# Optimization experiments

Hardware: AMD Instinct MI355X
Metric: run time of the kernel (lower is better)

## Reference

```python
import jax, jax.numpy as jnp
import numpy as np

B, P, C, H, W = 256, 512, 512, 7, 8
T = H * W  # 56
EPS = 1e-8


def setup_inputs() -> dict:
    key = jax.random.key(0)
    k1, k2, k3 = jax.random.split(key, 3)
    inp = jax.random.normal(k1, (B, C, H, W), dtype=jnp.float32)
    # xavier-uniform-like init for prototype (fan over last two dims as torch does)
    bound_p = float(np.sqrt(6.0 / (P + C * T)))
    prototype = jax.random.uniform(k2, (P, C, T), dtype=jnp.float32, minval=-bound_p, maxval=bound_p)
    bound_w = float(np.sqrt(6.0 / (C + 1)))
    fc_w = jax.random.uniform(k3, (1, C), dtype=jnp.float32, minval=-bound_w, maxval=bound_w)
    fc_b = jnp.zeros((1,), dtype=jnp.float32)
    return {"input": inp, "prototype": prototype, "fc_w": fc_w, "fc_b": fc_b}


def reference(input, prototype, fc_w, fc_b):
    # flatten spatial dims: (B, C, T)
    x = input.reshape(input.shape[0], input.shape[1], -1)
    # per-position cosine similarity over channel dim
    dots = jnp.einsum('bct,pct->bpt', x, prototype)          # (B, P, T)
    xn = jnp.linalg.norm(x, axis=1)                           # (B, T)
    pn = jnp.linalg.norm(prototype, axis=1)                   # (P, T)
    sim = dots / jnp.maximum(xn[:, None, :] * pn[None, :, :], EPS)
    att = jax.nn.softmax(sim, axis=-1)                        # (B, P, T)
    # attention-pooled elementwise product: (B, P, C)
    feat = jnp.einsum('bpt,bct,pct->bpc', att, x, prototype)
    # fc: Linear(C, 1) then relu, view to (B, P)
    out = jax.nn.relu(jnp.einsum('bpc,oc->bpo', feat, fc_w) + fc_b)
    return out.reshape(out.shape[0], out.shape[1])
```

## Files before the change

kernel.cpp:

```cpp
#include <hip/hip_runtime.h>
#include <hip/hip_bf16.h>
#include <math.h>

constexpr int kB = 256, kC = 512, kT = 56, kP = 512;
constexpr int kCT = kC * kT;

typedef short v4s __attribute__((ext_vector_type(4)));
typedef short v8s __attribute__((ext_vector_type(8)));
typedef float v4f __attribute__((ext_vector_type(4)));
typedef float v16f __attribute__((ext_vector_type(16)));

__device__ __forceinline__ unsigned pack_bf16(float a, float b) {
  __hip_bfloat16 ha = __float2bfloat16(a);
  __hip_bfloat16 hb = __float2bfloat16(b);
  unsigned short ua, ub;
  __builtin_memcpy(&ua, &ha, 2);
  __builtin_memcpy(&ub, &hb, 2);
  return (unsigned)ua | ((unsigned)ub << 16);
}

__device__ __forceinline__ v4s frag2(unsigned w0, unsigned w1) {
  unsigned u[2] = {w0, w1};
  v4s s;
  __builtin_memcpy(&s, u, 8);
  return s;
}

__device__ __forceinline__ v8s frag8(uint4 u) {
  v8s s;
  __builtin_memcpy(&s, &u, 16);
  return s;
}

__device__ __forceinline__ unsigned cvtpk(float lo, float hi) {
  unsigned r;
  asm("v_cvt_pk_bf16_f32 %0, %1, %2" : "=v"(r) : "v"(lo), "v"(hi));
  return r;
}

#define GLOAD(gp, lp)                                                        \
  __builtin_amdgcn_global_load_lds(                                          \
      (const __attribute__((address_space(1))) unsigned*)(const unsigned*)(gp), \
      (__attribute__((address_space(3))) unsigned*)(unsigned*)(lp), 16, 0, 0)


__global__ __launch_bounds__(512) void prep_kernel(
    const float* __restrict__ x, const float* __restrict__ proto,
    const float* __restrict__ fcw,
    unsigned* __restrict__ xt, unsigned* __restrict__ xwt,
    unsigned* __restrict__ pt,
    float* __restrict__ xn2, float* __restrict__ pn2) {
  __shared__ float tile[128 * 64];
  __shared__ float normp[56 * 16];

  const int tid = threadIdx.x;
  const int n = blockIdx.x;
  const bool isx = (n < kB);
  const int row = isx ? n : (n - kB);
  const float* src = (isx ? x : proto) + (size_t)row * kCT;
  const int R = isx ? kB : kP;
  unsigned* dst0 = isx ? xt : pt;

  const int l = tid & 63;
  const int w = tid >> 6;
  const int j = l & 15;
  const int tq = l >> 4;

  float na0 = 0.f, na1 = 0.f;

#pragma unroll 1
  for (int ch = 0; ch < 4; ++ch) {
    const float* csrc = src + ch * (128 * 56);

    float fw[8];
    if (isx) {
      const float* gf = fcw + ch * 128 + 8 * j;
#pragma unroll
      for (int i = 0; i < 8; ++i) fw[i] = gf[i];
    }

#pragma unroll
    for (int it = 0; it < 4; ++it) {
      const int idx = it * 512 + tid;
      if (idx < 1792) {
        const int f0 = idx * 4;
        const int c = (int)(((unsigned)f0 * 74899u) >> 22);
        const int t = f0 - c * 56;
        const int sw = ((((unsigned)c >> 3) ^ (unsigned)c) & 7) << 2;
        float4 v = *(const float4*)(csrc + f0);
        *(float4*)(tile + c * 64 + (t ^ sw)) = v;
      }
    }
    __syncthreads();

#pragma unroll
    for (int pass = 0; pass < 2; ++pass) {
      const int t = pass * 32 + w * 4 + tq;
      if (t < 56) {
        float f[8];
#pragma unroll
        for (int i = 0; i < 8; ++i) {
          const int sw = ((j ^ i) & 7) << 2;
          f[i] = tile[(8 * j + i) * 64 + (t ^ sw)];
        }
        float s = 0.f;
#pragma unroll
        for (int i = 0; i < 8; ++i) s = fmaf(f[i], f[i], s);
        if (pass == 0) na0 += s; else na1 += s;
        uint4 wx;
        wx.x = cvtpk(f[0], f[1]);
        wx.y = cvtpk(f[2], f[3]);
        wx.z = cvtpk(f[4], f[5]);
        wx.w = cvtpk(f[6], f[7]);
        const size_t o = (size_t)(t >> 2) * ((size_t)R * 1024) +
                         (size_t)row * 1024 + ch * 256 + (t & 3) * 64 + 4 * j;
        *(uint4*)(dst0 + o) = wx;
        if (isx) {
          uint4 ww;
          ww.x = cvtpk(f[0] * fw[0], f[1] * fw[1]);
          ww.y = cvtpk(f[2] * fw[2], f[3] * fw[3]);
          ww.z = cvtpk(f[4] * fw[4], f[5] * fw[5]);
          ww.w = cvtpk(f[6] * fw[6], f[7] * fw[7]);
          *(uint4*)(xwt + o) = ww;
        }
      }
    }
    __syncthreads();
  }

  {
    const int t0 = w * 4 + tq;
    normp[t0 * 16 + j] = na0;
    const int t1 = 32 + w * 4 + tq;
    if (t1 < 56) normp[t1 * 16 + j] = na1;
  }
  __syncthreads();
  if (tid < 56) {
    float s = 0.f;
#pragma unroll
    for (int k = 0; k < 16; ++k) s += normp[tid * 16 + k];
    if (isx) xn2[row * 56 + tid] = s;
    else     pn2[row * 56 + tid] = s;
  }
}

constexpr int TILE = 64 * 32;
constexpr int BUF = 3 * TILE;

__global__ __launch_bounds__(256, 2) void proto_gemm_kernel(
    const unsigned* __restrict__ xt, const unsigned* __restrict__ xwt,
    const unsigned* __restrict__ pt,
    const float* __restrict__ xn2, const float* __restrict__ pn2,
    float* __restrict__ part) {
  __shared__ __align__(16) unsigned lds[3 * BUF];
  __shared__ float xnL[4 * 64], pnL[4 * 64];

  const int tid = threadIdx.x;
  const int l = tid & 63;
  const int w4 = tid >> 6;
  const int wm = w4 >> 1;
  const int wn = w4 & 1;

  int bid = (int)blockIdx.x;
  bid = (bid & 7) * 56 + (bid >> 3);
  const int b0 = (bid & 3) * 64;
  const int p0 = ((bid >> 2) & 7) * 64;
  const int tg = bid >> 5;

  {
    const int tl = tid >> 6, r = tid & 63;
    xnL[tid] = sqrtf(xn2[(b0 + r) * 56 + tg * 4 + tl]);
    pnL[tid] = sqrtf(pn2[(p0 + r) * 56 + tg * 4 + tl]);
  }
  __syncthreads();

  const int lrow = l >> 3, lch = l & 7;
  size_t xsrc[2], psrc[2];
  int ldst[2];
#pragma unroll
  for (int j = 0; j < 2; ++j) {
    const int row = w4 * 16 + j * 8 + lrow;
    const int ch4 = ((lch ^ (row & 7))) * 4;
    xsrc[j] = (size_t)(b0 + row) * 1024 + ch4;
    psrc[j] = (size_t)(p0 + row) * 1024 + ch4;
    ldst[j] = (w4 * 16 + j * 8) * 32;
  }

  const int fr = l & 31;
  const int hi = l >> 5;
  const int axb = (wm * 32 + fr) * 32;
  const int pxb = (wn * 32 + fr) * 32;
  const int frs = fr & 7;

  v16f aD, aW, sac, nac;
#pragma unroll
  for (int i = 0; i < 16; ++i) { aD[i] = 0.f; aW[i] = 0.f; sac[i] = 0.f; nac[i] = 0.f; }

  auto STAGE = [&](int s, int buf) {
    const int t = tg * 4 + (s >> 3);
    const int kw = s & 7;
    const size_t base = (size_t)(t >> 2) * 1024 + (size_t)((t & 3) * 64) +
                        (size_t)((kw >> 1) * 256 + (kw & 1) * 32);
    const size_t xo = (size_t)(t >> 2) * ((size_t)kB * 1024 - 1024) + base;
    const size_t po = (size_t)(t >> 2) * ((size_t)kP * 1024 - 1024) + base;
    unsigned* lb = lds + buf * BUF;
#pragma unroll
    for (int j = 0; j < 2; ++j) {
      GLOAD(xt + xsrc[j] + xo, lb + ldst[j]);
      GLOAD(xwt + xsrc[j] + xo, lb + TILE + ldst[j]);
      GLOAD(pt + psrc[j] + po, lb + 2 * TILE + ldst[j]);
    }
  };

  auto COMPUTE = [&](int s, int buf) {
    const unsigned* bx = lds + buf * BUF;
#pragma unroll
    for (int ks = 0; ks < 4; ++ks) {
      const int col = (((ks << 1) | hi) ^ frs) << 2;
      v8s xf = frag8(*(const uint4*)(bx + axb + col));
      v8s wf = frag8(*(const uint4*)(bx + TILE + axb + col));
      v8s pf = frag8(*(const uint4*)(bx + 2 * TILE + pxb + col));
      aD = __builtin_amdgcn_mfma_f32_32x32x16_bf16(xf, pf, aD, 0, 0, 0);
      aW = __builtin_amdgcn_mfma_f32_32x32x16_bf16(wf, pf, aW, 0, 0, 0);
    }
    if ((s & 7) == 7) {
      const int tl = s >> 3;
      const float pnv = pnL[tl * 64 + wn * 32 + fr];
#pragma unroll
      for (int i = 0; i < 16; ++i) {
        const int drow = (i & 3) + 8 * (i >> 2) + 4 * hi;
        const float xnv = xnL[tl * 64 + wm * 32 + drow];
        float den = fmaxf(xnv * pnv, 1e-8f);
        float sim = aD[i] * __builtin_amdgcn_rcpf(den);
        float e = __expf(sim);
        sac[i] += e;
        nac[i] = fmaf(e, aW[i], nac[i]);
        aD[i] = 0.f;
        aW[i] = 0.f;
      }
    }
  };

  STAGE(0, 0);
  STAGE(1, 1);

  int c0 = 0, c1 = 1, c2 = 2;
#pragma unroll 1
  for (int s = 0; s < 32; ++s) {
    if (s < 31) asm volatile("s_waitcnt vmcnt(6)" ::: "memory");
    else        asm volatile("s_waitcnt vmcnt(0)" ::: "memory");
    __builtin_amdgcn_s_barrier();
    __builtin_amdgcn_sched_barrier(0);
    COMPUTE(s, c0);
    if (s < 30) STAGE(s + 2, c2);
    const int tmp = c0; c0 = c1; c1 = c2; c2 = tmp;
  }

  float* psb = part + ((size_t)tg * 2 + 0) * 131072;
  float* pnb = part + ((size_t)tg * 2 + 1) * 131072;
#pragma unroll
  for (int i = 0; i < 16; ++i) {
    const int drow = (i & 3) + 8 * (i >> 2) + 4 * hi;
    const size_t o = (size_t)(b0 + wm * 32 + drow) * 512 + p0 + wn * 32 + fr;
    psb[o] = sac[i];
    pnb[o] = nac[i];
  }
}

__global__ __launch_bounds__(256) void merge_kernel(
    const float* __restrict__ part, const float* __restrict__ fcb,
    float* __restrict__ out) {
  const int pair = blockIdx.x * 256 + threadIdx.x;
  float S = 0.f, N = 0.f;
#pragma unroll
  for (int k = 0; k < 14; ++k) {
    S += part[((size_t)k * 2 + 0) * 131072 + pair];
    N += part[((size_t)k * 2 + 1) * 131072 + pair];
  }
  float o = N * __builtin_amdgcn_rcpf(S) + fcb[0];
  out[pair] = fmaxf(o, 0.f);
}

__global__ __launch_bounds__(1024) void proto_mfma_kernel(
    const float* __restrict__ x, const float* __restrict__ proto,
    const float* __restrict__ fcw, const float* __restrict__ fcb,
    float* __restrict__ out) {
  __shared__ unsigned xs[56 * 289];
  __shared__ unsigned ps[56 * 145];
  __shared__ unsigned pws[56 * 145];

  const int tid = threadIdx.x;
  const int l = tid & 63;
  const int w = tid >> 6;
  const int bq = w & 1;
  const int tq = w >> 1;
  const int t0 = tq * 7;

  const int n = blockIdx.y * 32 + blockIdx.x;
  const int p0 = (n >> 3) * 16;
  const int b0 = (n & 7) * 32;

  const bool act = (l < 56);
  const int lt = l;

  const int xbase0 = ((b0 + 2 * w + 0) * kC) * kT + lt;
  const int xbase1 = ((b0 + 2 * w + 1) * kC) * kT + lt;
  const int pbase = ((p0 + w) * kC) * kT + lt;

  const int arow = l & 15;
  const int q2 = (l >> 4) << 1;
  const int xoff = (bq * 16 + arow) * 9 + q2;
  const int poff = arow * 9 + q2;

  v4f acc[7][2];
#pragma unroll
  for (int ti = 0; ti < 7; ++ti) {
    acc[ti][0] = v4f{0.f, 0.f, 0.f, 0.f};
    acc[ti][1] = v4f{0.f, 0.f, 0.f, 0.f};
  }
  float xn2a = 0.f, xn2b = 0.f, pn2 = 0.f;

#pragma unroll 1
  for (int st = 0; st < 32; ++st) {
    const int k0 = st * 16;
    if (act) {
#pragma unroll
      for (int r = 0; r < 16; ++r) {
        const int cw = r & 7;
        const int c = k0 + 2 * cw;
        const int ga = ((r >> 3) ? xbase1 : xbase0) + c * kT;
        float g0 = x[ga], g1 = x[ga + kT];
        if (r >> 3) xn2b = fmaf(g0, g0, fmaf(g1, g1, xn2b));
        else xn2a = fmaf(g0, g0, fmaf(g1, g1, xn2a));
        xs[lt * 289 + (2 * w + (r >> 3)) * 9 + cw] = pack_bf16(g0, g1);
      }
#pragma unroll
      for (int cw = 0; cw < 8; ++cw) {
        const int c = k0 + 2 * cw;
        const int ga = pbase + c * kT;
        float g0 = proto[ga], g1 = proto[ga + kT];
        pn2 = fmaf(g0, g0, fmaf(g1, g1, pn2));
        ps[lt * 145 + w * 9 + cw] = pack_bf16(g0, g1);
        float f0 = fcw[c], f1 = fcw[c + 1];
        pws[lt * 145 + w * 9 + cw] = pack_bf16(g0 * f0, g1 * f1);
      }
    }
    __syncthreads();
#pragma unroll
    for (int ti = 0; ti < 7; ++ti) {
      const int t = t0 + ti;
      unsigned xw0 = xs[t * 289 + xoff];
      unsigned xw1 = xs[t * 289 + xoff + 1];
      unsigned pw0 = ps[t * 145 + poff];
      unsigned pw1 = ps[t * 145 + poff + 1];
      unsigned ww0 = pws[t * 145 + poff];
      unsigned ww1 = pws[t * 145 + poff + 1];
      v4s af = frag2(xw0, xw1);
      v4s bf = frag2(pw0, pw1);
      v4s wf = frag2(ww0, ww1);
      acc[ti][0] = __builtin_amdgcn_mfma_f32_16x16x16bf16_1k(af, bf, acc[ti][0], 0, 0, 0);
      acc[ti][1] = __builtin_amdgcn_mfma_f32_16x16x16bf16_1k(af, wf, acc[ti][1], 0, 0, 0);
    }
    __syncthreads();
  }

  float* xnorm = (float*)ps;
  float* pnorm = xnorm + 32 * 56;
  if (act) {
    xnorm[(2 * w + 0) * 56 + lt] = xn2a;
    xnorm[(2 * w + 1) * 56 + lt] = xn2b;
    pnorm[w * 56 + lt] = pn2;
  }
  __syncthreads();

  float* fm = (float*)xs;
  float* fsum = fm + 4096;
  float* fnum = fsum + 4096;
  const int pc = arow;
  const int qq = l >> 4;
#pragma unroll
  for (int i = 0; i < 4; ++i) {
    const int bl = bq * 16 + 4 * qq + i;
    float m = -3.0e38f;
    float sims[7];
#pragma unroll
    for (int ti = 0; ti < 7; ++ti) {
      const int t = t0 + ti;
      float den = fmaxf(sqrtf(xnorm[bl * 56 + t]) * sqrtf(pnorm[pc * 56 + t]), 1e-8f);
      float s = acc[ti][0][i] / den;
      sims[ti] = s;
      m = fmaxf(m, s);
    }
    float se = 0.f, nu = 0.f;
#pragma unroll
    for (int ti = 0; ti < 7; ++ti) {
      float e = __expf(sims[ti] - m);
      se += e;
      nu = fmaf(e, acc[ti][1][i], nu);
    }
    const int pair = bl * 16 + pc;
    fm[tq * 512 + pair] = m;
    fsum[tq * 512 + pair] = se;
    fnum[tq * 512 + pair] = nu;
  }
  __syncthreads();

  if (tid < 512) {
    float M = -3.0e38f;
#pragma unroll
    for (int k = 0; k < 8; ++k) M = fmaxf(M, fm[k * 512 + tid]);
    float S = 0.f, N = 0.f;
#pragma unroll
    for (int k = 0; k < 8; ++k) {
      float sc = __expf(fm[k * 512 + tid] - M);
      S = fmaf(fsum[k * 512 + tid], sc, S);
      N = fmaf(fnum[k * 512 + tid], sc, N);
    }
    float o = N / S + fcb[0];
    out[(b0 + (tid >> 4)) * kP + p0 + (tid & 15)] = fmaxf(o, 0.f);
  }
}

extern "C" void kernel_launch(void* const* d_in, const int* in_sizes, int n_in,
                              void* d_out, int out_size, void* d_ws, size_t ws_size,
                              hipStream_t stream) {
  const float* x = (const float*)d_in[0];
  const float* proto = (const float*)d_in[1];
  const float* fcw = (const float*)d_in[2];
  const float* fcb = (const float*)d_in[3];
  float* out = (float*)d_out;

  const size_t need = 73572352;
  if (ws_size >= need) {
    unsigned* xt = (unsigned*)d_ws;
    unsigned* xwt = xt + 3670016;
    unsigned* ptb = xt + 7340032;
    float* partb = (float*)(xt + 14680064);
    float* xn2b = (float*)(xt + 18350080);
    float* pn2b = xn2b + 14336;

    hipLaunchKernelGGL(prep_kernel, dim3(kB + kP), dim3(512), 0, stream,
                       x, proto, fcw, xt, xwt, ptb, xn2b, pn2b);
    hipLaunchKernelGGL(proto_gemm_kernel, dim3(448), dim3(256), 0, stream,
                       xt, xwt, ptb, xn2b, pn2b, partb);
    hipLaunchKernelGGL(merge_kernel, dim3(512), dim3(256), 0, stream,
                       partb, fcb, out);
  } else {
    hipLaunchKernelGGL(proto_mfma_kernel, dim3(32, 8), dim3(1024), 0, stream,
                       x, proto, fcw, fcb, out);
  }
}
```

Baseline: 61.36 us.

## Fold fc weight into GEMM on the fly, drop xwt buffer, deepen LDS pipeline

Stops the prep kernel from writing a separate fc-weighted bf16 copy of x. The GEMM instead multiplies the loaded x fragment by the fc weights, held as packed bf16 in LDS, to form the second MFMA operand. This removes one global write stream in prep and one global load stream per stage in the GEMM. With smaller per-stage buffers the pipeline goes from 3 to 4 stages with adjusted vmcnt waits. The cost is extra VALU work per fragment and double bf16 rounding (x is rounded, then x*w is rounded again).

```diff
diff --git a/kernel.cpp b/kernel.cpp
--- a/kernel.cpp
+++ b/kernel.cpp
@@ -32,6 +32,18 @@
   return s;
 }
 
+__device__ __forceinline__ float bfl(unsigned u) {
+  unsigned v = u << 16;
+  float f;
+  __builtin_memcpy(&f, &v, 4);
+  return f;
+}
+__device__ __forceinline__ float bfh(unsigned u) {
+  unsigned v = u & 0xffff0000u;
+  float f;
+  __builtin_memcpy(&f, &v, 4);
+  return f;
+}
 __device__ __forceinline__ unsigned cvtpk(float lo, float hi) {
   unsigned r;
   asm("v_cvt_pk_bf16_f32 %0, %1, %2" : "=v"(r) : "v"(lo), "v"(hi));
@@ -46,9 +58,7 @@
 
 __global__ __launch_bounds__(512) void prep_kernel(
     const float* __restrict__ x, const float* __restrict__ proto,
-    const float* __restrict__ fcw,
-    unsigned* __restrict__ xt, unsigned* __restrict__ xwt,
-    unsigned* __restrict__ pt,
+    unsigned* __restrict__ xt, unsigned* __restrict__ pt,
     float* __restrict__ xn2, float* __restrict__ pn2) {
   __shared__ float tile[128 * 64];
   __shared__ float normp[56 * 16];
@@ -71,13 +81,6 @@
 #pragma unroll 1
   for (int ch = 0; ch < 4; ++ch) {
     const float* csrc = src + ch * (128 * 56);
-
-    float fw[8];
-    if (isx) {
-      const float* gf = fcw + ch * 128 + 8 * j;
-#pragma unroll
-      for (int i = 0; i < 8; ++i) fw[i] = gf[i];
-    }
 
 #pragma unroll
     for (int it = 0; it < 4; ++it) {
@@ -115,14 +118,6 @@
         const size_t o = (size_t)(t >> 2) * ((size_t)R * 1024) +
                          (size_t)row * 1024 + ch * 256 + (t & 3) * 64 + 4 * j;
         *(uint4*)(dst0 + o) = wx;
-        if (isx) {
-          uint4 ww;
-          ww.x = cvtpk(f[0] * fw[0], f[1] * fw[1]);
-          ww.y = cvtpk(f[2] * fw[2], f[3] * fw[3]);
-          ww.z = cvtpk(f[4] * fw[4], f[5] * fw[5]);
-          ww.w = cvtpk(f[6] * fw[6], f[7] * fw[7]);
-          *(uint4*)(xwt + o) = ww;
-        }
       }
     }
     __syncthreads();
@@ -145,14 +140,15 @@
 }
 
 constexpr int TILE = 64 * 32;
-constexpr int BUF = 3 * TILE;
+constexpr int BUF = 2 * TILE;
 
 __global__ __launch_bounds__(256, 2) void proto_gemm_kernel(
-    const unsigned* __restrict__ xt, const unsigned* __restrict__ xwt,
-    const unsigned* __restrict__ pt,
+    const unsigned* __restrict__ xt, const unsigned* __restrict__ pt,
+    const float* __restrict__ fcw,
     const float* __restrict__ xn2, const float* __restrict__ pn2,
     float* __restrict__ part) {
-  __shared__ __align__(16) unsigned lds[3 * BUF];
+  __shared__ __align__(16) unsigned lds[4 * BUF];
+  __shared__ unsigned fcwL[256];
   __shared__ float xnL[4 * 64], pnL[4 * 64];
 
   const int tid = threadIdx.x;
@@ -171,6 +167,7 @@
     const int tl = tid >> 6, r = tid & 63;
     xnL[tid] = sqrtf(xn2[(b0 + r) * 56 + tg * 4 + tl]);
     pnL[tid] = sqrtf(pn2[(p0 + r) * 56 + tg * 4 + tl]);
+    fcwL[tid] = pack_bf16(fcw[2 * tid], fcw[2 * tid + 1]);
   }
   __syncthreads();
 
@@ -199,27 +196,34 @@
   auto STAGE = [&](int s, int buf) {
     const int t = tg * 4 + (s >> 3);
     const int kw = s & 7;
-    const size_t base = (size_t)(t >> 2) * 1024 + (size_t)((t & 3) * 64) +
+    const size_t base = (size_t)((t & 3) * 64) +
                         (size_t)((kw >> 1) * 256 + (kw & 1) * 32);
-    const size_t xo = (size_t)(t >> 2) * ((size_t)kB * 1024 - 1024) + base;
-    const size_t po = (size_t)(t >> 2) * ((size_t)kP * 1024 - 1024) + base;
+    const size_t xo = (size_t)(t >> 2) * ((size_t)kB * 1024) + base;
+    const size_t po = (size_t)(t >> 2) * ((size_t)kP * 1024) + base;
     unsigned* lb = lds + buf * BUF;
 #pragma unroll
     for (int j = 0; j < 2; ++j) {
       GLOAD(xt + xsrc[j] + xo, lb + ldst[j]);
-      GLOAD(xwt + xsrc[j] + xo, lb + TILE + ldst[j]);
-      GLOAD(pt + psrc[j] + po, lb + 2 * TILE + ldst[j]);
+      GLOAD(pt + psrc[j] + po, lb + TILE + ldst[j]);
     }
   };
 
   auto COMPUTE = [&](int s, int buf) {
     const unsigned* bx = lds + buf * BUF;
+    const int kw = s & 7;
 #pragma unroll
     for (int ks = 0; ks < 4; ++ks) {
-      const int col = (((ks << 1) | hi) ^ frs) << 2;
-      v8s xf = frag8(*(const uint4*)(bx + axb + col));
-      v8s wf = frag8(*(const uint4*)(bx + TILE + axb + col));
-      v8s pf = frag8(*(const uint4*)(bx + 2 * TILE + pxb + col));
+      const int q = (ks << 1) | hi;
+      const int col = (q ^ frs) << 2;
+      uint4 xr = *(const uint4*)(bx + axb + col);
+      uint4 pr = *(const uint4*)(bx + TILE + pxb + col);
+      uint4 fw = *(const uint4*)(fcwL + kw * 32 + (q << 2));
+      uint4 wr;
+      wr.x = cvtpk(bfl(xr.x) * bfl(fw.x), bfh(xr.x) * bfh(fw.x));
+      wr.y = cvtpk(bfl(xr.y) * bfl(fw.y), bfh(xr.y) * bfh(fw.y));
+      wr.z = cvtpk(bfl(xr.z) * bfl(fw.z), bfh(xr.z) * bfh(fw.z));
+      wr.w = cvtpk(bfl(xr.w) * bfl(fw.w), bfh(xr.w) * bfh(fw.w));
+      v8s xf = frag8(xr), wf = frag8(wr), pf = frag8(pr);
       aD = __builtin_amdgcn_mfma_f32_32x32x16_bf16(xf, pf, aD, 0, 0, 0);
       aW = __builtin_amdgcn_mfma_f32_32x32x16_bf16(wf, pf, aW, 0, 0, 0);
     }
@@ -243,17 +247,17 @@
 
   STAGE(0, 0);
   STAGE(1, 1);
-
-  int c0 = 0, c1 = 1, c2 = 2;
+  STAGE(2, 2);
+
 #pragma unroll 1
   for (int s = 0; s < 32; ++s) {
-    if (s < 31) asm volatile("s_waitcnt vmcnt(6)" ::: "memory");
-    else        asm volatile("s_waitcnt vmcnt(0)" ::: "memory");
+    if (s < 30)      asm volatile("s_waitcnt vmcnt(8)" ::: "memory");
+    else if (s == 30) asm volatile("s_waitcnt vmcnt(4)" ::: "memory");
+    else              asm volatile("s_waitcnt vmcnt(0)" ::: "memory");
     __builtin_amdgcn_s_barrier();
     __builtin_amdgcn_sched_barrier(0);
-    COMPUTE(s, c0);
-    if (s < 30) STAGE(s + 2, c2);
-    const int tmp = c0; c0 = c1; c1 = c2; c2 = tmp;
+    COMPUTE(s, s & 3);
+    if (s < 29) STAGE(s + 3, (s + 3) & 3);
   }
 
   float* psb = part + ((size_t)tg * 2 + 0) * 131072;
@@ -433,16 +437,15 @@
   const size_t need = 73572352;
   if (ws_size >= need) {
     unsigned* xt = (unsigned*)d_ws;
-    unsigned* xwt = xt + 3670016;
     unsigned* ptb = xt + 7340032;
     float* partb = (float*)(xt + 14680064);
     float* xn2b = (float*)(xt + 18350080);
     float* pn2b = xn2b + 14336;
 
     hipLaunchKernelGGL(prep_kernel, dim3(kB + kP), dim3(512), 0, stream,
-                       x, proto, fcw, xt, xwt, ptb, xn2b, pn2b);
+                       x, proto, xt, ptb, xn2b, pn2b);
     hipLaunchKernelGGL(proto_gemm_kernel, dim3(448), dim3(256), 0, stream,
-                       xt, xwt, ptb, xn2b, pn2b, partb);
+                       xt, ptb, fcw, xn2b, pn2b, partb);
     hipLaunchKernelGGL(merge_kernel, dim3(512), dim3(256), 0, stream,
                        partb, fcb, out);
   } else {
```

New measurement: 64.23 us. 1.05x slower.
